# Optimization experiments

Measured on AMD Instinct MI355X. Metric: run time of the kernel, lower is better.

Reference implementation:

```python
import jax, jax.numpy as jnp
import numpy as np

D = 1024      # embed_dim
E = 2048      # expand * embed_dim
S_DIM = 128   # shrunken attn dim s
C = 256       # chunk size
SRC = 4096    # src_len
G = SRC // C  # num chunks
B = 8
STD = 0.02


def setup_inputs() -> dict:
    key = jax.random.key(0)
    ks = jax.random.split(key, 16)
    n = lambda k, shp: jax.random.normal(k, shp, dtype=jnp.float32)
    inp = {
        "query": n(ks[0], (SRC, B, D)),
        "key":   n(ks[1], (SRC, B, D)),
        "value": n(ks[2], (SRC, B, D)),
        # learned params (torch Linear stored as [in, out])
        "Wxs": n(ks[3], (D, S_DIM)) * STD, "bxs": n(ks[4], (S_DIM,)) * STD,
        "Wve": n(ks[5], (D, E)) * STD,     "bve": n(ks[6], (E,)) * STD,
        "Wue": n(ks[7], (D, E)) * STD,     "bue": n(ks[8], (E,)) * STD,
        "Wod": n(ks[9], (E, D)) * STD,     "bod": n(ks[10], (D,)) * STD,
        "rel_bias": n(ks[11], (C,)) * STD,
        "gamma": n(ks[12], (4, S_DIM)) * STD,
        "beta":  n(ks[13], (4, S_DIM)) * STD,
    }
    return inp


def reference(query, key, value, Wxs, bxs, Wve, bve, Wue, bue, Wod, bod,
              rel_bias, gamma, beta):
    # [S, B, D] -> [B, G, C, D]
    x = jnp.transpose(value, (1, 0, 2)).reshape(B, G, C, D)
    v = jnp.tanh(x @ Wve + bve)          # [b,g,c,e]
    z = jnp.tanh(x @ Wxs + bxs)          # [b,g,c,s]
    q_quad = z * gamma[0] + beta[0]
    k_quad = z * gamma[1] + beta[1]
    q_lin  = z * gamma[2] + beta[2]
    k_lin  = z * gamma[3] + beta[3]
    # local quadratic attention: relu(qk + bias)^2
    qk = jnp.einsum('bgns,bgms->bgnm', q_quad, k_quad)
    a = jnp.square(jax.nn.relu(qk + rel_bias))
    v_quad = jnp.einsum('bgnm,bgme->bgne', a, v)
    # global linear attention
    kv = jnp.einsum('bgcs,bgce->bse', k_lin, v)
    v_lin = jnp.einsum('bgcs,bse->bgce', q_lin, kv)
    u = jnp.tanh(x @ Wue + bue)          # [b,g,c,e]
    o = (u * (v_quad + v_lin)) @ Wod + bod   # [b,g,c,d]
    o = o.reshape(B, G * C, D)
    return jnp.transpose(o, (1, 0, 2))   # [S, B, D]
```

## Files before the change

### kernel.cpp

```cpp
#include <hip/hip_runtime.h>
#include <hip/hip_bf16.h>

using u16 = unsigned short;
using u32 = unsigned int;

typedef __attribute__((ext_vector_type(8))) short bf8;
typedef __attribute__((ext_vector_type(4))) float f4;
typedef __attribute__((ext_vector_type(4))) u16  us4;

#define DEV static __device__ __forceinline__

DEV float bf2f(u16 u) { return __uint_as_float(((u32)u) << 16); }
DEV u16 f2bf(float f) {
    u32 x = __float_as_uint(f);
    x += 0x7FFFu + ((x >> 16) & 1u);
    return (u16)(x >> 16);
}
DEV float tanhf_fast(float x) {
    float e = __expf(2.0f * x);
    return 1.0f - 2.0f / (e + 1.0f);
}
DEV f4 MFMA(bf8 a, bf8 b, f4 c) {
    return __builtin_amdgcn_mfma_f32_16x16x32_bf16(a, b, c, 0, 0, 0);
}
DEV int xcd_swz(int bx, int nwg) { return (bx & 7) * (nwg >> 3) + (bx >> 3); }

DEV void gload16(const u16* src, u16* dst) {
    __builtin_amdgcn_global_load_lds(
        (const __attribute__((address_space(1))) void*)src,
        (__attribute__((address_space(3))) void*)dst, 16, 0, 0);
}


#define WS_XB    ((size_t)0)
#define WS_WXST  ((size_t)67108864)
#define WS_WVET  ((size_t)67371008)
#define WS_WUET  ((size_t)71565312)
#define WS_WODT  ((size_t)75759616)
#define WS_KVT   ((size_t)79953920)
#define WS_A     ((size_t)84148224)
#define WS_QL    ((size_t)100925440)
#define WS_VT    ((size_t)109314048)
#define WS_T1    ((size_t)243531776)
#define WS_Z     ((size_t)243531776)
#define WS_KLT   ((size_t)251920384)
#define WS_QQ    ((size_t)260308992)
#define WS_KQ    ((size_t)268697600)
#define WS_KVF   ((size_t)277086208)

DEV void stage128x64(const u16* __restrict__ gbase, int ld, u16* lds, int w, int lane) {
    const int srow = lane >> 3;
    const int scol = ((lane & 7) ^ srow) * 8;
    #pragma unroll
    for (int i = 0; i < 4; i++) {
        const int rt = (i * 4 + w) * 8 + srow;
        const u16* src = gbase + (size_t)rt * ld + scol;
        u16* dst = lds + (size_t)(i * 4 + w) * 512;
        gload16(src, dst);
    }
}

DEV void frag_mfma_64_swz(const u16* As, const u16* Bs, int wm, int wn, int ln, int lh,
                          f4 acc[4][4]) {
    #pragma unroll
    for (int kk2 = 0; kk2 < 2; kk2++) {
        const int sx = (((kk2 << 2) + lh) ^ (ln & 7)) << 3;
        bf8 a[4], b[4];
        #pragma unroll
        for (int mt = 0; mt < 4; mt++)
            a[mt] = *reinterpret_cast<const bf8*>(As + (wm * 64 + mt * 16 + ln) * 64 + sx);
        #pragma unroll
        for (int nt = 0; nt < 4; nt++)
            b[nt] = *reinterpret_cast<const bf8*>(Bs + (wn * 64 + nt * 16 + ln) * 64 + sx);
        #pragma unroll
        for (int mt = 0; mt < 4; mt++)
            #pragma unroll
            for (int nt = 0; nt < 4; nt++)
                acc[mt][nt] = MFMA(a[mt], b[nt], acc[mt][nt]);
    }
}

template<int NT, typename FA, typename FB>
DEV void gemm_pipe(FA stageA, FB stageB, u16* As, u16* Bs,
                   int wm, int wn, int ln, int lh, f4 acc[4][4]) {
    stageA(As, 0); stageB(Bs, 0);
    #pragma unroll 2
    for (int t = 0; t + 1 < NT; ++t) {
        u16* An = As + ((t & 1) ^ 1) * 8192;
        u16* Bn = Bs + ((t & 1) ^ 1) * 8192;
        stageA(An, t + 1); stageB(Bn, t + 1);
        asm volatile("s_waitcnt vmcnt(8)" ::: "memory");
        __builtin_amdgcn_s_barrier();
        __builtin_amdgcn_sched_barrier(0);
        frag_mfma_64_swz(As + (t & 1) * 8192, Bs + (t & 1) * 8192, wm, wn, ln, lh, acc);
        __builtin_amdgcn_sched_barrier(0);
        __builtin_amdgcn_s_barrier();
        __builtin_amdgcn_sched_barrier(0);
    }
    asm volatile("s_waitcnt vmcnt(0)" ::: "memory");
    __builtin_amdgcn_s_barrier();
    frag_mfma_64_swz(As + ((NT - 1) & 1) * 8192, Bs + ((NT - 1) & 1) * 8192, wm, wn, ln, lh, acc);
    __builtin_amdgcn_s_barrier();
}


#define T256 16384

DEV void stage256x64(const u16* __restrict__ gbase, int ld, u16* lds, int tid) {
    const int slot = tid & 7;
    #pragma unroll
    for (int i = 0; i < 4; i++) {
        const int row = i * 64 + (tid >> 3);
        const u16* src = gbase + (size_t)row * ld + ((slot ^ (row & 7)) << 3);
        u16* dst = lds + ((size_t)(i * 512 + (tid & ~63)) << 3);
        gload16(src, dst);
    }
}

DEV void tile_mfma256(const u16* As, const u16* Bs, int wm, int wn, int ln, int lh,
                      f4 acc[8][4]) {
    __builtin_amdgcn_s_setprio(1);
    #pragma unroll
    for (int p = 0; p < 4; p++) {
        const int mg = p >> 1, ks = p & 1;
        const int sx = (((ks << 2) + lh) ^ (ln & 7)) << 3;
        bf8 a[4], b[4];
        #pragma unroll
        for (int j = 0; j < 4; j++)
            a[j] = *reinterpret_cast<const bf8*>(As + (wm * 128 + (mg * 4 + j) * 16 + ln) * 64 + sx);
        #pragma unroll
        for (int n = 0; n < 4; n++)
            b[n] = *reinterpret_cast<const bf8*>(Bs + (wn * 64 + n * 16 + ln) * 64 + sx);
        #pragma unroll
        for (int j = 0; j < 4; j++)
            #pragma unroll
            for (int n = 0; n < 4; n++)
                acc[mg * 4 + j][n] = MFMA(a[j], b[n], acc[mg * 4 + j][n]);
        __builtin_amdgcn_sched_barrier(0);
    }
    __builtin_amdgcn_s_setprio(0);
}

template<int NT, typename F>
DEV void gemm_pipe256(F stage, u16* As, u16* Bs, int wm, int wn, int ln, int lh,
                      f4 acc[8][4]) {
    stage(As, Bs, 0);
    #pragma unroll 2
    for (int t = 0; t + 1 < NT; ++t) {
        const int cur = t & 1, nxt = cur ^ 1;
        stage(As + nxt * T256, Bs + nxt * T256, t + 1);
        asm volatile("s_waitcnt vmcnt(8)" ::: "memory");
        __builtin_amdgcn_s_barrier();
        __builtin_amdgcn_sched_barrier(0);
        tile_mfma256(As + cur * T256, Bs + cur * T256, wm, wn, ln, lh, acc);
        __builtin_amdgcn_sched_barrier(0);
        __builtin_amdgcn_s_barrier();
        __builtin_amdgcn_sched_barrier(0);
    }
    asm volatile("s_waitcnt vmcnt(0)" ::: "memory");
    __builtin_amdgcn_s_barrier();
    tile_mfma256(As + ((NT - 1) & 1) * T256, Bs + ((NT - 1) & 1) * T256, wm, wn, ln, lh, acc);
    __builtin_amdgcn_s_barrier();
}

__global__ void k_cvt_x(const float* __restrict__ src, u16* __restrict__ dst) {
    int m = blockIdx.x;
    int s = m >> 3, b = m & 7;
    const float* in = src + (size_t)m * 1024;
    u16* outp = dst + (((size_t)b << 12) + s) * 1024;
    int t = threadIdx.x * 4;
    float4 v = *reinterpret_cast<const float4*>(in + t);
    us4 o; o[0] = f2bf(v.x); o[1] = f2bf(v.y); o[2] = f2bf(v.z); o[3] = f2bf(v.w);
    *reinterpret_cast<us4*>(outp + t) = o;
}

__global__ void k_transpose(const float* __restrict__ src, u16* __restrict__ dst, int R, int C) {
    __shared__ u16 tile[32][33];
    int tx = threadIdx.x & 31, ty = threadIdx.x >> 5;
    int r0 = blockIdx.y * 32, c0 = blockIdx.x * 32;
    #pragma unroll
    for (int rr = ty; rr < 32; rr += 8)
        tile[rr][tx] = f2bf(src[(size_t)(r0 + rr) * C + c0 + tx]);
    __syncthreads();
    #pragma unroll
    for (int cc = ty; cc < 32; cc += 8)
        dst[(size_t)(c0 + cc) * R + r0 + tx] = tile[tx][cc];
}

__global__ void k_klinT(const u16* __restrict__ z, const float* __restrict__ gamma,
                        const float* __restrict__ beta, u16* __restrict__ klt) {
    __shared__ u16 tile[32][33];
    int tx = threadIdx.x & 31, ty = threadIdx.x >> 5;
    int r0 = blockIdx.x * 32;
    int c0 = blockIdx.y * 32;
    float gs = gamma[384 + c0 + tx], bs = beta[384 + c0 + tx];
    #pragma unroll
    for (int rr = ty; rr < 32; rr += 8) {
        u16 zv = z[(size_t)(r0 + rr) * 128 + c0 + tx];
        tile[rr][tx] = f2bf(bf2f(zv) * gs + bs);
    }
    __syncthreads();
    int b = r0 >> 12;
    int pos0 = r0 & 4095;
    #pragma unroll
    for (int cc = ty; cc < 32; cc += 8)
        klt[(((size_t)b * 128 + c0 + cc) << 12) + pos0 + tx] = tile[tx][cc];
}

__global__ __launch_bounds__(256) void k_zgemm(const u16* __restrict__ xb, const u16* __restrict__ WxsT,
                                               const float* __restrict__ bxs,
                                               const float* __restrict__ gamma, const float* __restrict__ beta,
                                               u16* __restrict__ z, u16* __restrict__ qq,
                                               u16* __restrict__ kq, u16* __restrict__ ql) {
    __shared__ u16 As[2][128 * 64];
    __shared__ u16 Bs[2][128 * 64];
    const int tid = threadIdx.x;
    const int lane = tid & 63, w = tid >> 6;
    const int ln = lane & 15, lh = lane >> 4;
    const int wm = w >> 1, wn = w & 1;
    const int rowbase = xcd_swz(blockIdx.x, 256) * 128;
    const u16* Ab = xb + (size_t)rowbase * 1024;
    f4 acc[4][4] = {};
    gemm_pipe<16>(
        [&](u16* l, int t) { stage128x64(Ab + t * 64, 1024, l, w, lane); },
        [&](u16* l, int t) { stage128x64(WxsT + t * 64, 1024, l, w, lane); },
        As[0], Bs[0], wm, wn, ln, lh, acc);
    #pragma unroll
    for (int mt = 0; mt < 4; mt++)
        #pragma unroll
        for (int nt = 0; nt < 4; nt++) {
            int col = wn * 64 + nt * 16 + ln;
            float bias = bxs[col];
            float g0 = gamma[col],       b0 = beta[col];
            float g1 = gamma[128 + col], b1 = beta[128 + col];
            float g2 = gamma[256 + col], b2 = beta[256 + col];
            int r0 = rowbase + wm * 64 + mt * 16 + lh * 4;
            #pragma unroll
            for (int rg = 0; rg < 4; rg++) {
                float zv = tanhf_fast(acc[mt][nt][rg] + bias);
                size_t idx = ((size_t)(r0 + rg) << 7) + col;
                z[idx]  = f2bf(zv);
                qq[idx] = f2bf(zv * g0 + b0);
                kq[idx] = f2bf(zv * g1 + b1);
                ql[idx] = f2bf(zv * g2 + b2);
            }
        }
}

__global__ __launch_bounds__(512, 2) void k_vgemm(const u16* __restrict__ xb, const u16* __restrict__ WveT,
                                                  const float* __restrict__ bve, u16* __restrict__ vT) {
    __shared__ u16 As[2 * T256];
    __shared__ u16 Bs[2 * T256];
    const int tid = threadIdx.x;
    const int lane = tid & 63, w = tid >> 6;
    const int ln = lane & 15, lh = lane >> 4;
    const int wm = w >> 2, wn = w & 3;
    const int rowbase = xcd_swz(blockIdx.x, 128) * 256;
    const int colbase = blockIdx.y * 256;
    const u16* Ab = xb + (size_t)rowbase * 1024;
    const u16* Bb = WveT + (size_t)colbase * 1024;
    f4 acc[8][4] = {};
    gemm_pipe256<16>(
        [&](u16* a, u16* b, int t) {
            stage256x64(Ab + t * 64, 1024, a, tid);
            stage256x64(Bb + t * 64, 1024, b, tid);
        },
        As, Bs, wm, wn, ln, lh, acc);
    #pragma unroll
    for (int mt = 0; mt < 8; mt++)
        #pragma unroll
        for (int nt = 0; nt < 4; nt++) {
            int e = colbase + wn * 64 + nt * 16 + ln;
            float bias = bve[e];
            int r0 = rowbase + wm * 128 + mt * 16 + lh * 4;
            int bb = r0 >> 12, s0 = r0 & 4095;
            us4 p;
            #pragma unroll
            for (int rg = 0; rg < 4; rg++) p[rg] = f2bf(tanhf_fast(acc[mt][nt][rg] + bias));
            *reinterpret_cast<us4*>(vT + (((size_t)bb * 2048 + e) << 12) + s0) = p;
        }
}

__global__ __launch_bounds__(256) void k_kv(const u16* __restrict__ vT, const u16* __restrict__ klt,
                                            float* __restrict__ kvF) {
    __shared__ u16 As[2][128 * 64];
    __shared__ u16 Bs[2][128 * 64];
    const int tid = threadIdx.x;
    const int lane = tid & 63, w = tid >> 6;
    const int ln = lane & 15, lh = lane >> 4;
    const int wm = w >> 1, wn = w & 1;
    const int b = blockIdx.z;
    const int rowbase = blockIdx.x * 128;
    const int kbase = blockIdx.y * 1024;
    const u16* Ab = vT + ((size_t)b * 2048 + rowbase) * 4096 + kbase;
    const u16* Bb = klt + ((size_t)b * 128) * 4096 + kbase;
    f4 acc[4][4] = {};
    gemm_pipe<16>(
        [&](u16* l, int t) { stage128x64(Ab + t * 64, 4096, l, w, lane); },
        [&](u16* l, int t) { stage128x64(Bb + t * 64, 4096, l, w, lane); },
        As[0], Bs[0], wm, wn, ln, lh, acc);
    #pragma unroll
    for (int mt = 0; mt < 4; mt++)
        #pragma unroll
        for (int nt = 0; nt < 4; nt++) {
            int s = wn * 64 + nt * 16 + ln;
            int e0 = rowbase + wm * 64 + mt * 16 + lh * 4;
            #pragma unroll
            for (int rg = 0; rg < 4; rg++)
                atomicAdd(&kvF[(((size_t)b * 2048 + e0 + rg) << 7) + s], acc[mt][nt][rg]);
        }
}

__global__ void k_kvcvt(const float* __restrict__ kvF, u16* __restrict__ kvT, int n) {
    int i = (blockIdx.x * blockDim.x + threadIdx.x) * 4;
    if (i < n) {
        float4 v = *reinterpret_cast<const float4*>(kvF + i);
        us4 o; o[0] = f2bf(v.x); o[1] = f2bf(v.y); o[2] = f2bf(v.z); o[3] = f2bf(v.w);
        *reinterpret_cast<us4*>(kvT + i) = o;
    }
}

__global__ __launch_bounds__(256) void k_a(const u16* __restrict__ qq, const u16* __restrict__ kq,
                                           const float* __restrict__ rel_bias, u16* __restrict__ a_out) {
    const int lane = threadIdx.x & 63, wid = threadIdx.x >> 6;
    const int ln = lane & 15, lh = lane >> 4;
    const int wm = wid >> 1, wn = wid & 1;
    const int ci = blockIdx.y;
    const int qbase = blockIdx.x * 128 + wm * 64;
    const int nbase = wn * 128;
    const int rowbase = ci << 8;
    f4 acc[4][8] = {};
    const u16* qr[4];
    #pragma unroll
    for (int mt = 0; mt < 4; mt++) qr[mt] = qq + ((size_t)(rowbase + qbase + mt * 16 + ln) << 7);
    const u16* kr[8];
    #pragma unroll
    for (int nt = 0; nt < 8; nt++) kr[nt] = kq + ((size_t)(rowbase + nbase + nt * 16 + ln) << 7);
    #pragma unroll
    for (int kk = 0; kk < 128; kk += 32) {
        int k0 = kk + lh * 8;
        bf8 aq[4], ak[8];
        #pragma unroll
        for (int mt = 0; mt < 4; mt++) aq[mt] = *reinterpret_cast<const bf8*>(qr[mt] + k0);
        #pragma unroll
        for (int nt = 0; nt < 8; nt++) ak[nt] = *reinterpret_cast<const bf8*>(kr[nt] + k0);
        #pragma unroll
        for (int mt = 0; mt < 4; mt++)
            #pragma unroll
            for (int nt = 0; nt < 8; nt++)
                acc[mt][nt] = MFMA(aq[mt], ak[nt], acc[mt][nt]);
    }
    #pragma unroll
    for (int nt = 0; nt < 8; nt++) {
        int key = nbase + nt * 16 + ln;
        float rb = rel_bias[key];
        #pragma unroll
        for (int mt = 0; mt < 4; mt++) {
            int r0 = qbase + mt * 16 + lh * 4;
            #pragma unroll
            for (int rg = 0; rg < 4; rg++) {
                float v = acc[mt][nt][rg] + rb;
                v = fmaxf(v, 0.0f); v = v * v;
                a_out[((size_t)ci << 16) + ((size_t)(r0 + rg) << 8) + key] = f2bf(v);
            }
        }
    }
}

__global__ __launch_bounds__(512, 2) void k_t1(const u16* __restrict__ ql, const u16* __restrict__ a_in,
                                               const u16* __restrict__ vT, const u16* __restrict__ kvT,
                                               u16* __restrict__ t1) {
    __shared__ u16 As[2 * T256];
    __shared__ u16 Bs[2 * T256];
    const int tid = threadIdx.x;
    const int lane = tid & 63, w = tid >> 6;
    const int ln = lane & 15, lh = lane >> 4;
    const int wm = w >> 2, wn = w & 3;
    const int ci = xcd_swz(blockIdx.x, 128);
    const int rowbase = ci << 8;
    const int ebase = blockIdx.y * 256;
    const int b = ci >> 4, g = ci & 15;
    const u16* Aa = ql + (size_t)rowbase * 128;
    const u16* Ba = kvT + ((size_t)(b * 2048 + ebase)) * 128;
    const u16* Ab = a_in + ((size_t)ci << 16);
    const u16* Bb = vT + ((size_t)(b * 2048 + ebase)) * 4096 + (g << 8);
    f4 acc[8][4] = {};
    gemm_pipe256<6>(
        [&](u16* a, u16* bl, int t) {
            if (t < 2) {
                stage256x64(Aa + t * 64, 128, a, tid);
                stage256x64(Ba + t * 64, 128, bl, tid);
            } else {
                stage256x64(Ab + (t - 2) * 64, 256, a, tid);
                stage256x64(Bb + (t - 2) * 64, 4096, bl, tid);
            }
        },
        As, Bs, wm, wn, ln, lh, acc);
    #pragma unroll
    for (int mt = 0; mt < 8; mt++)
        #pragma unroll
        for (int nt = 0; nt < 4; nt++) {
            int e = ebase + wn * 64 + nt * 16 + ln;
            int r0 = rowbase + wm * 128 + mt * 16 + lh * 4;
            #pragma unroll
            for (int rg = 0; rg < 4; rg++)
                t1[((size_t)(r0 + rg) << 11) + e] = f2bf(acc[mt][nt][rg]);
        }
}

__global__ __launch_bounds__(512, 2) void k_u(const u16* __restrict__ xb, const u16* __restrict__ WueT,
                                              const float* __restrict__ bue, u16* t1) {
    __shared__ u16 As[2 * T256];
    __shared__ u16 Bs[2 * T256];
    const int tid = threadIdx.x;
    const int lane = tid & 63, w = tid >> 6;
    const int ln = lane & 15, lh = lane >> 4;
    const int wm = w >> 2, wn = w & 3;
    const int rowbase = xcd_swz(blockIdx.x, 128) * 256;
    const int colbase = blockIdx.y * 256;
    const u16* Ab = xb + (size_t)rowbase * 1024;
    const u16* Bb = WueT + (size_t)colbase * 1024;
    f4 acc[8][4] = {};
    gemm_pipe256<16>(
        [&](u16* a, u16* b, int t) {
            stage256x64(Ab + t * 64, 1024, a, tid);
            stage256x64(Bb + t * 64, 1024, b, tid);
        },
        As, Bs, wm, wn, ln, lh, acc);
    #pragma unroll
    for (int mt = 0; mt < 8; mt++)
        #pragma unroll
        for (int nt = 0; nt < 4; nt++) {
            int e = colbase + wn * 64 + nt * 16 + ln;
            float bias = bue[e];
            int r0 = rowbase + wm * 128 + mt * 16 + lh * 4;
            #pragma unroll
            for (int rg = 0; rg < 4; rg++) {
                size_t idx = ((size_t)(r0 + rg) << 11) + e;
                float t = bf2f(t1[idx]);
                float u = tanhf_fast(acc[mt][nt][rg] + bias);
                t1[idx] = f2bf(u * t);
            }
        }
}

__global__ __launch_bounds__(512, 2) void k_o(const u16* __restrict__ t1, const u16* __restrict__ WodT,
                                              const float* __restrict__ bod, float* __restrict__ out) {
    __shared__ u16 As[2 * T256];
    __shared__ u16 Bs[2 * T256];
    const int tid = threadIdx.x;
    const int lane = tid & 63, w = tid >> 6;
    const int ln = lane & 15, lh = lane >> 4;
    const int wm = w >> 2, wn = w & 3;
    const int rowbase = xcd_swz(blockIdx.x, 128) * 256;
    const int colbase = blockIdx.y * 256;
    const u16* Ab = t1 + (size_t)rowbase * 2048;
    const u16* Bb = WodT + (size_t)colbase * 2048;
    f4 acc[8][4] = {};
    gemm_pipe256<32>(
        [&](u16* a, u16* b, int t) {
            stage256x64(Ab + t * 64, 2048, a, tid);
            stage256x64(Bb + t * 64, 2048, b, tid);
        },
        As, Bs, wm, wn, ln, lh, acc);
    #pragma unroll
    for (int mt = 0; mt < 8; mt++)
        #pragma unroll
        for (int nt = 0; nt < 4; nt++) {
            int d = colbase + wn * 64 + nt * 16 + ln;
            float bias = bod[d];
            int r0 = rowbase + wm * 128 + mt * 16 + lh * 4;
            #pragma unroll
            for (int rg = 0; rg < 4; rg++) {
                int r = r0 + rg;
                int s = r & 4095, bb = r >> 12;
                out[((size_t)(s * 8 + bb) << 10) + d] = acc[mt][nt][rg] + bias;
            }
        }
}

extern "C" void kernel_launch(void* const* d_in, const int* in_sizes, int n_in,
                              void* d_out, int out_size, void* d_ws, size_t ws_size,
                              hipStream_t stream) {
    const float* value = (const float*)d_in[2];
    const float* Wxs = (const float*)d_in[3];  const float* bxs = (const float*)d_in[4];
    const float* Wve = (const float*)d_in[5];  const float* bve = (const float*)d_in[6];
    const float* Wue = (const float*)d_in[7];  const float* bue = (const float*)d_in[8];
    const float* Wod = (const float*)d_in[9];  const float* bod = (const float*)d_in[10];
    const float* rel_bias = (const float*)d_in[11];
    const float* gamma = (const float*)d_in[12];
    const float* beta  = (const float*)d_in[13];
    float* out = (float*)d_out;

    char* ws = (char*)d_ws;
    u16* xb   = (u16*)(ws + WS_XB);
    u16* WxsT = (u16*)(ws + WS_WXST);
    u16* WveT = (u16*)(ws + WS_WVET);
    u16* WueT = (u16*)(ws + WS_WUET);
    u16* WodT = (u16*)(ws + WS_WODT);
    u16* kvT  = (u16*)(ws + WS_KVT);
    u16* a    = (u16*)(ws + WS_A);
    u16* ql   = (u16*)(ws + WS_QL);
    u16* vT   = (u16*)(ws + WS_VT);
    u16* t1   = (u16*)(ws + WS_T1);
    u16* z    = (u16*)(ws + WS_Z);
    u16* klt  = (u16*)(ws + WS_KLT);
    u16* qq   = (u16*)(ws + WS_QQ);
    u16* kq   = (u16*)(ws + WS_KQ);
    float* kvF = (float*)(ws + WS_KVF);

    k_cvt_x<<<32768, 256, 0, stream>>>(value, xb);
    k_transpose<<<dim3(4, 32),  256, 0, stream>>>(Wxs, WxsT, 1024, 128);
    k_transpose<<<dim3(64, 32), 256, 0, stream>>>(Wve, WveT, 1024, 2048);
    k_transpose<<<dim3(64, 32), 256, 0, stream>>>(Wue, WueT, 1024, 2048);
    k_transpose<<<dim3(32, 64), 256, 0, stream>>>(Wod, WodT, 2048, 1024);
    k_zgemm<<<256, 256, 0, stream>>>(xb, WxsT, bxs, gamma, beta, z, qq, kq, ql);
    k_klinT<<<dim3(1024, 4), 256, 0, stream>>>(z, gamma, beta, klt);
    k_vgemm<<<dim3(128, 8), 512, 0, stream>>>(xb, WveT, bve, vT);
    hipMemsetAsync(kvF, 0, (size_t)8 * 2048 * 128 * 4, stream);
    k_kv<<<dim3(16, 4, 8), 256, 0, stream>>>(vT, klt, kvF);
    k_kvcvt<<<2048, 256, 0, stream>>>(kvF, kvT, 8 * 2048 * 128);
    k_a<<<dim3(2, 128), 256, 0, stream>>>(qq, kq, rel_bias, a);
    k_t1<<<dim3(128, 8), 512, 0, stream>>>(ql, a, vT, kvT, t1);
    k_u<<<dim3(128, 8), 512, 0, stream>>>(xb, WueT, bue, t1);
    k_o<<<dim3(128, 4), 512, 0, stream>>>(t1, WodT, bod, out);
}
```

Before: 768.8 us.

## Restructure 256-tile GEMM pipeline to prefetch two tiles ahead

Rewrites the double-buffered 256x256 GEMM main loop so both LDS buffers are filled before the loop starts. Each iteration loads all fragments for a k-half, then reissues the global-to-LDS stage for tile t+2 into the buffer just consumed, placed between barriers in the middle of the compute. The aim is to keep more global loads in flight and overlap them with MFMA work instead of waiting at the top of each iteration. The cost is more register pressure from holding 8 A and 4 B fragments at once, plus a tighter barrier and waitcnt ordering that must stay correct.

```diff
diff --git a/kernel.cpp b/kernel.cpp
--- a/kernel.cpp
+++ b/kernel.cpp
@@ -117,50 +117,66 @@
     }
 }
 
-DEV void tile_mfma256(const u16* As, const u16* Bs, int wm, int wn, int ln, int lh,
-                      f4 acc[8][4]) {
-    __builtin_amdgcn_s_setprio(1);
-    #pragma unroll
-    for (int p = 0; p < 4; p++) {
-        const int mg = p >> 1, ks = p & 1;
-        const int sx = (((ks << 2) + lh) ^ (ln & 7)) << 3;
-        bf8 a[4], b[4];
-        #pragma unroll
-        for (int j = 0; j < 4; j++)
-            a[j] = *reinterpret_cast<const bf8*>(As + (wm * 128 + (mg * 4 + j) * 16 + ln) * 64 + sx);
-        #pragma unroll
-        for (int n = 0; n < 4; n++)
-            b[n] = *reinterpret_cast<const bf8*>(Bs + (wn * 64 + n * 16 + ln) * 64 + sx);
-        #pragma unroll
-        for (int j = 0; j < 4; j++)
-            #pragma unroll
-            for (int n = 0; n < 4; n++)
-                acc[mg * 4 + j][n] = MFMA(a[j], b[n], acc[mg * 4 + j][n]);
-        __builtin_amdgcn_sched_barrier(0);
-    }
-    __builtin_amdgcn_s_setprio(0);
+DEV const bf8* frag_ptr(const u16* base, int row, int ks, int lh) {
+    const int slot = ((ks << 2) + lh) ^ (row & 7);
+    return reinterpret_cast<const bf8*>(base + row * 64 + slot * 8);
 }
 
 template<int NT, typename F>
 DEV void gemm_pipe256(F stage, u16* As, u16* Bs, int wm, int wn, int ln, int lh,
                       f4 acc[8][4]) {
     stage(As, Bs, 0);
+    if (NT > 1) stage(As + T256, Bs + T256, 1);
+    asm volatile("s_waitcnt vmcnt(8)" ::: "memory");
+    __builtin_amdgcn_s_barrier();
+    __builtin_amdgcn_sched_barrier(0);
     #pragma unroll 2
-    for (int t = 0; t + 1 < NT; ++t) {
-        const int cur = t & 1, nxt = cur ^ 1;
-        stage(As + nxt * T256, Bs + nxt * T256, t + 1);
-        asm volatile("s_waitcnt vmcnt(8)" ::: "memory");
-        __builtin_amdgcn_s_barrier();
-        __builtin_amdgcn_sched_barrier(0);
-        tile_mfma256(As + cur * T256, Bs + cur * T256, wm, wn, ln, lh, acc);
-        __builtin_amdgcn_sched_barrier(0);
-        __builtin_amdgcn_s_barrier();
-        __builtin_amdgcn_sched_barrier(0);
-    }
-    asm volatile("s_waitcnt vmcnt(0)" ::: "memory");
-    __builtin_amdgcn_s_barrier();
-    tile_mfma256(As + ((NT - 1) & 1) * T256, Bs + ((NT - 1) & 1) * T256, wm, wn, ln, lh, acc);
-    __builtin_amdgcn_s_barrier();
+    for (int t = 0; t < NT; ++t) {
+        const int cur = t & 1;
+        const u16* Ab = As + cur * T256;
+        const u16* Bb = Bs + cur * T256;
+        {
+            bf8 a[8], b[4];
+            #pragma unroll
+            for (int mt = 0; mt < 8; mt++) a[mt] = *frag_ptr(Ab, wm * 128 + mt * 16 + ln, 0, lh);
+            #pragma unroll
+            for (int nt = 0; nt < 4; nt++) b[nt] = *frag_ptr(Bb, wn * 64 + nt * 16 + ln, 0, lh);
+            __builtin_amdgcn_s_setprio(1);
+            #pragma unroll
+            for (int mt = 0; mt < 8; mt++)
+                #pragma unroll
+                for (int nt = 0; nt < 4; nt++)
+                    acc[mt][nt] = MFMA(a[mt], b[nt], acc[mt][nt]);
+            __builtin_amdgcn_s_setprio(0);
+        }
+        {
+            bf8 a[8], b[4];
+            #pragma unroll
+            for (int mt = 0; mt < 8; mt++) a[mt] = *frag_ptr(Ab, wm * 128 + mt * 16 + ln, 1, lh);
+            #pragma unroll
+            for (int nt = 0; nt < 4; nt++) b[nt] = *frag_ptr(Bb, wn * 64 + nt * 16 + ln, 1, lh);
+            asm volatile("s_waitcnt lgkmcnt(0)" ::: "memory");
+            __builtin_amdgcn_sched_barrier(0);
+            __builtin_amdgcn_s_barrier();
+            __builtin_amdgcn_sched_barrier(0);
+            if (t + 2 < NT) {
+                stage(As + cur * T256, Bs + cur * T256, t + 2);
+                asm volatile("s_waitcnt vmcnt(8)" ::: "memory");
+            } else {
+                asm volatile("s_waitcnt vmcnt(0)" ::: "memory");
+            }
+            __builtin_amdgcn_s_barrier();
+            __builtin_amdgcn_sched_barrier(0);
+            __builtin_amdgcn_s_setprio(1);
+            #pragma unroll
+            for (int mt = 0; mt < 8; mt++)
+                #pragma unroll
+                for (int nt = 0; nt < 4; nt++)
+                    acc[mt][nt] = MFMA(a[mt], b[nt], acc[mt][nt]);
+            __builtin_amdgcn_s_setprio(0);
+            __builtin_amdgcn_sched_barrier(0);
+        }
+    }
 }
 
 __global__ void k_cvt_x(const float* __restrict__ src, u16* __restrict__ dst) {
```

Result: slower. 920.9 us (+19.8%).
